# Optimization experiments

Hardware: AMD Instinct MI355X
Metric: run time of the kernel (lower is better)

## Reference

```python
import jax, jax.numpy as jnp
import numpy as np

BATCH = 1024
D_IN = 4096
D_OUT = 4096
B = 128  # block size
K_IN = (D_IN + B - 1) // B    # 32
K_OUT = (D_OUT + B - 1) // B  # 32


def setup_inputs() -> dict:
    key = jax.random.key(0)
    kx, kw, kd = jax.random.split(key, 3)
    x = jax.random.normal(kx, (BATCH, D_IN), dtype=jnp.float32)
    W = jax.random.normal(kw, (K_OUT, K_IN, B), dtype=jnp.float32) * 0.1
    # Bernoulli +/-1 diagonal
    D_bernoulli = jnp.where(jax.random.bernoulli(kd, p=0.5, shape=(D_IN,)), 1.0, -1.0).astype(jnp.float32)
    return {"x": x, "W": W, "D_bernoulli": D_bernoulli}


def reference(x, W, D_bernoulli):
    k_out, k_in, b = W.shape
    d_in = D_IN
    d_out = D_OUT
    if x.ndim == 1:
        x = x[None, :]
    batch = x.shape[0]
    # diagonal sign flip
    x_d = x * D_bernoulli[None, :]
    pad_len = k_in * b - d_in
    if pad_len > 0:
        x_d = jnp.pad(x_d, ((0, 0), (0, pad_len)))
    x_blocks = x_d.reshape(batch, k_in, b)
    # frequency-domain block-circulant matmul
    X_fft = jnp.fft.fft(x_blocks, axis=-1)            # (batch, k_in, b) complex
    W_fft = jnp.fft.fft(W, axis=-1)                    # (k_out, k_in, b) complex
    # Y_fft[n,o,:] = sum_j X_fft[n,j,:] * conj(W_fft[o,j,:])
    Y_fft = jnp.einsum('njb,ojb->nob', X_fft, jnp.conjugate(W_fft))
    Y = jnp.fft.ifft(Y_fft, axis=-1).real              # (batch, k_out, b)
    out_flat = Y.reshape(batch, k_out * b)
    if k_out * b > d_out:
        out_flat = out_flat[:, :d_out]
    return out_flat
```

## Files before the change

kernel.cpp:

```cpp
#include <hip/hip_runtime.h>
#include <hip/hip_bf16.h>

#define BATCH 1024
#define NF    65
#define TWOPI_OVER_B 0.049087385212340517f

typedef __attribute__((ext_vector_type(8))) short bf16x8;
typedef __attribute__((ext_vector_type(4))) float f32x4;

static __device__ __forceinline__ unsigned short f2bf(float f) {
    __hip_bfloat16 h = __float2bfloat16(f);
    return *reinterpret_cast<unsigned short*>(&h);
}
static __device__ __forceinline__ unsigned long long pack4(float a, float b, float c, float d) {
    return (unsigned long long)f2bf(a) | ((unsigned long long)f2bf(b) << 16)
         | ((unsigned long long)f2bf(c) << 32) | ((unsigned long long)f2bf(d) << 48);
}

__global__ __launch_bounds__(256) void k_init_frag(unsigned short* __restrict__ fragB,
                                                   unsigned short* __restrict__ fragCi) {
    int i = blockIdx.x * 256 + threadIdx.x;
    if (i < 18432) {
        int e = i & 7, l = (i >> 3) & 63, kb = (i >> 9) & 3, c = i >> 11;
        int kr = c * 16 + (l & 15);
        int t  = kb * 32 + (l >> 4) * 8 + e;
        float v = 0.f;
        if (kr < 65)       v =  cosf(TWOPI_OVER_B * (float)((kr * t) & 127));
        else if (kr < 130) v = -sinf(TWOPI_OVER_B * (float)(((kr - 65) * t) & 127));
        fragB[i] = f2bf(v);
    }
    if (i < 20480) {
        int e = i & 7, l = (i >> 3) & 63;
        int ckb = i >> 9; int kb = ckb % 5, c = ckb / 5;
        int kr = kb * 32 + (l >> 4) * 8 + e;
        int t  = c * 16 + (l & 15);
        float v = 0.f;
        if (kr < 65)       v =  cosf(TWOPI_OVER_B * (float)((kr * t) & 127));
        else if (kr < 130) v = -sinf(TWOPI_OVER_B * (float)(((kr - 65) * t) & 127));
        fragCi[i] = f2bf(v);
    }
}

#define SMEM_A_BYTES 37120

__global__ __launch_bounds__(256) void k_fdft_mfma(const float* __restrict__ x,
                                                   const float* __restrict__ D,
                                                   const bf16x8* __restrict__ fragB,
                                                   unsigned short* __restrict__ Xb) {
    __shared__ char smem[SMEM_A_BYTES];
    unsigned long long* xs8 = (unsigned long long*)smem;
    float* Yl = (float*)smem;
    int tid = threadIdx.x;
    int n0 = blockIdx.x * 2;

    #pragma unroll
    for (int it = 0; it < 8; ++it) {
        int f  = tid + it * 256;
        int nn = f >> 10;
        int f4 = f & 1023;
        float4 xa = ((const float4*)(x + (size_t)(n0 + nn) * 4096))[f4];
        float4 da = ((const float4*)D)[f4];
        int rl = nn * 32 + (f4 >> 5);
        int t0 = (f4 & 31) * 4;
        unsigned long long pk = pack4(xa.x * da.x, xa.y * da.y, xa.z * da.z, xa.w * da.w);
        int byte = (rl * 256 + t0 * 2) ^ ((rl & 7) << 4);
        xs8[byte >> 3] = pk;
    }
    __syncthreads();

    int l = tid & 63, w = tid >> 6;
    int rl_a = w * 16 + (l & 15);
    int coff = (l >> 4) * 16;
    bf16x8 a[4];
    #pragma unroll
    for (int kb = 0; kb < 4; ++kb) {
        int byte = (rl_a * 256 + kb * 64 + coff) ^ ((rl_a & 7) << 4);
        a[kb] = *(const bf16x8*)(smem + byte);
    }
    f32x4 acc[9];
    #pragma unroll
    for (int c = 0; c < 9; ++c) acc[c] = (f32x4)0.f;
    #pragma unroll
    for (int c = 0; c < 9; ++c)
        #pragma unroll
        for (int kb = 0; kb < 4; ++kb)
            acc[c] = __builtin_amdgcn_mfma_f32_16x16x32_bf16(a[kb], fragB[(c * 4 + kb) * 64 + l], acc[c], 0, 0, 0);
    __syncthreads();

    int rowd = w * 16 + (l >> 4) * 4;
    int cold = l & 15;
    #pragma unroll
    for (int c = 0; c < 9; ++c)
        #pragma unroll
        for (int r = 0; r < 4; ++r)
            Yl[(rowd + r) * 145 + c * 16 + cold] = acc[c][r];
    __syncthreads();

    for (int c2 = tid; c2 < 2080; c2 += 256) {
        int k = c2 >> 5, sub = c2 & 31, nn = sub >> 4, t = sub & 15;
        int j0 = t * 4;
        int col = (j0 < 32) ? k : 65 + k;
        int rlb = nn * 32 + (j0 & 31);
        unsigned long long pk = pack4(Yl[(rlb + 0) * 145 + col], Yl[(rlb + 1) * 145 + col],
                                      Yl[(rlb + 2) * 145 + col], Yl[(rlb + 3) * 145 + col]);
        *(unsigned long long*)(Xb + ((size_t)k * 1024 + n0 + nn) * 64 + j0) = pk;
    }
}

__global__ __launch_bounds__(256) void k_wfs_mfma(const float* __restrict__ W,
                                                  const bf16x8* __restrict__ fragB,
                                                  unsigned short* __restrict__ BmatT) {
    __shared__ char smem[SMEM_A_BYTES];
    unsigned long long* xs8 = (unsigned long long*)smem;
    float* Yl = (float*)smem;
    int tid = threadIdx.x;
    int o0 = blockIdx.x * 2;

    #pragma unroll
    for (int it = 0; it < 8; ++it) {
        int f  = tid + it * 256;
        float4 wa = ((const float4*)W)[(size_t)blockIdx.x * 2048 + f];
        int rl = f >> 5;
        int t0 = (f & 31) * 4;
        unsigned long long pk = pack4(wa.x, wa.y, wa.z, wa.w);
        int byte = (rl * 256 + t0 * 2) ^ ((rl & 7) << 4);
        xs8[byte >> 3] = pk;
    }
    __syncthreads();

    int l = tid & 63, w = tid >> 6;
    int rl_a = w * 16 + (l & 15);
    int coff = (l >> 4) * 16;
    bf16x8 a[4];
    #pragma unroll
    for (int kb = 0; kb < 4; ++kb) {
        int byte = (rl_a * 256 + kb * 64 + coff) ^ ((rl_a & 7) << 4);
        a[kb] = *(const bf16x8*)(smem + byte);
    }
    f32x4 acc[9];
    #pragma unroll
    for (int c = 0; c < 9; ++c) acc[c] = (f32x4)0.f;
    #pragma unroll
    for (int c = 0; c < 9; ++c)
        #pragma unroll
        for (int kb = 0; kb < 4; ++kb)
            acc[c] = __builtin_amdgcn_mfma_f32_16x16x32_bf16(a[kb], fragB[(c * 4 + kb) * 64 + l], acc[c], 0, 0, 0);
    __syncthreads();

    int rowd = w * 16 + (l >> 4) * 4;
    int cold = l & 15;
    #pragma unroll
    for (int c = 0; c < 9; ++c)
        #pragma unroll
        for (int r = 0; r < 4; ++r)
            Yl[(rowd + r) * 145 + c * 16 + cold] = acc[c][r];
    __syncthreads();

    for (int c2 = tid; c2 < 4160; c2 += 256) {
        int k = c2 >> 6, sub = c2 & 63;
        int oo = sub >> 5, h = (sub >> 4) & 1, t = sub & 15;
        int j0 = t * 4;
        float sc = (k == 0 || k == 64) ? (1.f / 128.f) : (2.f / 128.f);
        int col; float sgn;
        if (j0 < 32) { col = h ? 65 + k : k;  sgn = h ? -sc : sc; }
        else         { col = h ? k : 65 + k;  sgn = sc; }
        int rlb = oo * 32 + (j0 & 31);
        unsigned long long pk = pack4(sgn * Yl[(rlb + 0) * 145 + col], sgn * Yl[(rlb + 1) * 145 + col],
                                      sgn * Yl[(rlb + 2) * 145 + col], sgn * Yl[(rlb + 3) * 145 + col]);
        int o2 = h * 32 + o0 + oo;
        *(unsigned long long*)(BmatT + ((size_t)k * 64 + o2) * 64 + j0) = pk;
    }
}

__global__ __launch_bounds__(256) void k_einsum_mfma(const unsigned short* __restrict__ Xb,
                                                     const unsigned short* __restrict__ BmatT,
                                                     unsigned short* __restrict__ Y2) {
    __shared__ char lds[16384];
    int tid = threadIdx.x, l = tid & 63, w = tid >> 6;
    int k = blockIdx.x >> 3, mt = blockIdx.x & 7;
    int m0 = mt * 128 + w * 32;
    int lr = l & 15, lq = l >> 4;

    bf16x8 a[2][2], b[4][2];
    #pragma unroll
    for (int rf = 0; rf < 2; ++rf)
        #pragma unroll
        for (int kb = 0; kb < 2; ++kb)
            a[rf][kb] = *(const bf16x8*)(Xb + ((size_t)k * 1024 + m0 + rf * 16 + lr) * 64 + kb * 32 + lq * 8);
    #pragma unroll
    for (int cf = 0; cf < 4; ++cf)
        #pragma unroll
        for (int kb = 0; kb < 2; ++kb)
            b[cf][kb] = *(const bf16x8*)(BmatT + ((size_t)k * 64 + cf * 16 + lr) * 64 + kb * 32 + lq * 8);

    f32x4 acc[2][4];
    #pragma unroll
    for (int rf = 0; rf < 2; ++rf)
        #pragma unroll
        for (int cf = 0; cf < 4; ++cf) acc[rf][cf] = (f32x4)0.f;
    #pragma unroll
    for (int rf = 0; rf < 2; ++rf)
        #pragma unroll
        for (int cf = 0; cf < 4; ++cf) {
            acc[rf][cf] = __builtin_amdgcn_mfma_f32_16x16x32_bf16(a[rf][0], b[cf][0], acc[rf][cf], 0, 0, 0);
            acc[rf][cf] = __builtin_amdgcn_mfma_f32_16x16x32_bf16(a[rf][1], b[cf][1], acc[rf][cf], 0, 0, 0);
        }

    #pragma unroll
    for (int rf = 0; rf < 2; ++rf)
        #pragma unroll
        for (int cf = 0; cf < 4; ++cf)
            #pragma unroll
            for (int rr = 0; rr < 4; ++rr) {
                int row = rf * 16 + lq * 4 + rr;
                int col = cf * 16 + lr;
                int byte = w * 4096 + ((row * 128 + col * 2) ^ ((row & 7) << 4));
                *(unsigned short*)(lds + byte) = f2bf(acc[rf][cf][rr]);
            }
    __syncthreads();
    #pragma unroll
    for (int i = 0; i < 4; ++i) {
        int row = i * 8 + (l >> 3);
        int byte = w * 4096 + ((row * 128 + (l & 7) * 16) ^ ((row & 7) << 4));
        bf16x8 v = *(const bf16x8*)(lds + byte);
        *(bf16x8*)(Y2 + ((size_t)k * 1024 + m0 + row) * 64 + (l & 7) * 8) = v;
    }
}

__global__ __launch_bounds__(256) void k_idft_mfma(const unsigned short* __restrict__ Y2,
                                                   const bf16x8* __restrict__ fragCi,
                                                   float* __restrict__ out) {
    __shared__ char smem[20480];
    int tid = threadIdx.x;
    int row0 = blockIdx.x * 64;
    int n0 = blockIdx.x * 2;

    for (int i = tid; i < 1920; i += 256) {
        int rl = i / 30, cp = 130 + i % 30;
        int byte = (rl * 320 + cp * 2) ^ ((rl & 7) << 4);
        *(unsigned short*)(smem + byte) = 0;
    }
    for (int c2 = tid; c2 < 2080; c2 += 256) {
        int k = c2 >> 5, sub = c2 & 31, nn = sub >> 4, t = sub & 15;
        unsigned long long v = *(const unsigned long long*)(Y2 + ((size_t)k * 1024 + n0 + nn) * 64 + t * 4);
        int o2_0 = t * 4;
        int col = (o2_0 < 32) ? k : 65 + k;
        int r0 = nn * 32 + (o2_0 & 31);
        #pragma unroll
        for (int i = 0; i < 4; ++i) {
            int rl = r0 + i;
            int byte = (rl * 320 + col * 2) ^ ((rl & 7) << 4);
            *(unsigned short*)(smem + byte) = (unsigned short)(v >> (16 * i));
        }
    }
    __syncthreads();

    int l = tid & 63, w = tid >> 6;
    int rl_a = w * 16 + (l & 15);
    int coff = (l >> 4) * 16;
    bf16x8 a[5];
    #pragma unroll
    for (int kb = 0; kb < 5; ++kb) {
        int byte = (rl_a * 320 + kb * 64 + coff) ^ ((rl_a & 7) << 4);
        a[kb] = *(const bf16x8*)(smem + byte);
    }
    f32x4 acc[8];
    #pragma unroll
    for (int c = 0; c < 8; ++c) acc[c] = (f32x4)0.f;
    #pragma unroll
    for (int c = 0; c < 8; ++c)
        #pragma unroll
        for (int kb = 0; kb < 5; ++kb)
            acc[c] = __builtin_amdgcn_mfma_f32_16x16x32_bf16(a[kb], fragCi[(c * 5 + kb) * 64 + l], acc[c], 0, 0, 0);

    int rowd = row0 + w * 16 + (l >> 4) * 4;
    int cold = l & 15;
    #pragma unroll
    for (int c = 0; c < 8; ++c)
        #pragma unroll
        for (int r = 0; r < 4; ++r)
            out[(size_t)(rowd + r) * 128 + c * 16 + cold] = acc[c][r];
}

extern "C" void kernel_launch(void* const* d_in, const int* in_sizes, int n_in,
                              void* d_out, int out_size, void* d_ws, size_t ws_size,
                              hipStream_t stream) {
    const float* x = (const float*)d_in[0];
    const float* W = (const float*)d_in[1];
    const float* D = (const float*)d_in[2];
    float* out = (float*)d_out;
    float* ws  = (float*)d_ws;

    unsigned short* BmatT  = (unsigned short*)ws;
    unsigned short* Xb     = (unsigned short*)(ws + 133120);
    unsigned short* Y2     = (unsigned short*)(ws + 2263040);
    unsigned short* fragB  = (unsigned short*)(ws + 4392960);
    unsigned short* fragCi = (unsigned short*)(ws + 4402176);

    k_init_frag  <<<80, 256, 0, stream>>>(fragB, fragCi);
    k_wfs_mfma   <<<16, 256, 0, stream>>>(W, (const bf16x8*)fragB, BmatT);
    k_fdft_mfma  <<<512, 256, 0, stream>>>(x, D, (const bf16x8*)fragB, Xb);
    k_einsum_mfma<<<520, 256, 0, stream>>>(Xb, BmatT, Y2);
    k_idft_mfma  <<<512, 256, 0, stream>>>(Y2, (const bf16x8*)fragCi, out);
}
```

Measured before the change: 47.58 us.

## Fuse forward DFT, spectral einsum and inverse DFT into one kernel

```diff
diff --git a/kernel.cpp b/kernel.cpp
--- a/kernel.cpp
+++ b/kernel.cpp
@@ -1,8 +1,6 @@
 #include <hip/hip_runtime.h>
 #include <hip/hip_bf16.h>
 
-#define BATCH 1024
-#define NF    65
 #define TWOPI_OVER_B 0.049087385212340517f
 
 typedef __attribute__((ext_vector_type(8))) short bf16x8;
@@ -17,54 +15,59 @@
          | ((unsigned long long)f2bf(c) << 32) | ((unsigned long long)f2bf(d) << 48);
 }
 
-__global__ __launch_bounds__(256) void k_init_frag(unsigned short* __restrict__ fragB,
-                                                   unsigned short* __restrict__ fragCi) {
-    int i = blockIdx.x * 256 + threadIdx.x;
-    if (i < 18432) {
-        int e = i & 7, l = (i >> 3) & 63, kb = (i >> 9) & 3, c = i >> 11;
-        int kr = c * 16 + (l & 15);
-        int t  = kb * 32 + (l >> 4) * 8 + e;
+__global__ __launch_bounds__(256) void k_prep(const float* __restrict__ W,
+                                              unsigned short* __restrict__ fragB,
+                                              unsigned short* __restrict__ fragCi,
+                                              unsigned short* __restrict__ BmatT) {
+    __shared__ char smem[73984];
+    int tid = threadIdx.x;
+
+    if (blockIdx.x < 80) {
+        int i = blockIdx.x * 256 + tid;
+        if (i < 18432) {
+            int e = i & 7, l2 = (i >> 3) & 63, kb = (i >> 9) & 3, c = i >> 11;
+            int kr = c * 16 + (l2 & 15);
+            int t  = kb * 32 + (l2 >> 4) * 8 + e;
+            float v = 0.f;
+            if (kr < 65)       v =  cosf(TWOPI_OVER_B * (float)((kr * t) & 127));
+            else if (kr < 130) v = -sinf(TWOPI_OVER_B * (float)(((kr - 65) * t) & 127));
+            fragB[i] = f2bf(v);
+        }
+        if (i < 20480) {
+            int e = i & 7, l2 = (i >> 3) & 63;
+            int ckb = i >> 9; int kb = ckb % 5, c = ckb / 5;
+            int kr = kb * 32 + (l2 >> 4) * 8 + e;
+            int t  = c * 16 + (l2 & 15);
+            float v = 0.f;
+            if (kr < 65)       v =  cosf(TWOPI_OVER_B * (float)((kr * t) & 127));
+            else if (kr < 130) v = -sinf(TWOPI_OVER_B * (float)(((kr - 65) * t) & 127));
+            fragCi[i] = f2bf(v);
+        }
+        return;
+    }
+
+    int bw = blockIdx.x - 80;
+    unsigned long long* xs8 = (unsigned long long*)smem;
+    float* Yl = (float*)smem;
+    unsigned short* fB = (unsigned short*)(smem + 37120);
+
+    for (int i = tid; i < 18432; i += 256) {
+        int e = i & 7, l2 = (i >> 3) & 63, kb = (i >> 9) & 3, c = i >> 11;
+        int kr = c * 16 + (l2 & 15);
+        int t  = kb * 32 + (l2 >> 4) * 8 + e;
         float v = 0.f;
         if (kr < 65)       v =  cosf(TWOPI_OVER_B * (float)((kr * t) & 127));
         else if (kr < 130) v = -sinf(TWOPI_OVER_B * (float)(((kr - 65) * t) & 127));
-        fragB[i] = f2bf(v);
-    }
-    if (i < 20480) {
-        int e = i & 7, l = (i >> 3) & 63;
-        int ckb = i >> 9; int kb = ckb % 5, c = ckb / 5;
-        int kr = kb * 32 + (l >> 4) * 8 + e;
-        int t  = c * 16 + (l & 15);
-        float v = 0.f;
-        if (kr < 65)       v =  cosf(TWOPI_OVER_B * (float)((kr * t) & 127));
-        else if (kr < 130) v = -sinf(TWOPI_OVER_B * (float)(((kr - 65) * t) & 127));
-        fragCi[i] = f2bf(v);
-    }
-}
-
-#define SMEM_A_BYTES 37120
-
-__global__ __launch_bounds__(256) void k_fdft_mfma(const float* __restrict__ x,
-                                                   const float* __restrict__ D,
-                                                   const bf16x8* __restrict__ fragB,
-                                                   unsigned short* __restrict__ Xb) {
-    __shared__ char smem[SMEM_A_BYTES];
-    unsigned long long* xs8 = (unsigned long long*)smem;
-    float* Yl = (float*)smem;
-    int tid = threadIdx.x;
-    int n0 = blockIdx.x * 2;
-
+        fB[i] = f2bf(v);
+    }
     #pragma unroll
     for (int it = 0; it < 8; ++it) {
         int f  = tid + it * 256;
-        int nn = f >> 10;
-        int f4 = f & 1023;
-        float4 xa = ((const float4*)(x + (size_t)(n0 + nn) * 4096))[f4];
-        float4 da = ((const float4*)D)[f4];
-        int rl = nn * 32 + (f4 >> 5);
-        int t0 = (f4 & 31) * 4;
-        unsigned long long pk = pack4(xa.x * da.x, xa.y * da.y, xa.z * da.z, xa.w * da.w);
+        float4 wa = ((const float4*)W)[(size_t)bw * 2048 + f];
+        int rl = f >> 5;
+        int t0 = (f & 31) * 4;
         int byte = (rl * 256 + t0 * 2) ^ ((rl & 7) << 4);
-        xs8[byte >> 3] = pk;
+        xs8[byte >> 3] = pack4(wa.x, wa.y, wa.z, wa.w);
     }
     __syncthreads();
 
@@ -77,6 +80,8 @@
         int byte = (rl_a * 256 + kb * 64 + coff) ^ ((rl_a & 7) << 4);
         a[kb] = *(const bf16x8*)(smem + byte);
     }
+    __syncthreads();
+
     f32x4 acc[9];
     #pragma unroll
     for (int c = 0; c < 9; ++c) acc[c] = (f32x4)0.f;
@@ -84,8 +89,7 @@
     for (int c = 0; c < 9; ++c)
         #pragma unroll
         for (int kb = 0; kb < 4; ++kb)
-            acc[c] = __builtin_amdgcn_mfma_f32_16x16x32_bf16(a[kb], fragB[(c * 4 + kb) * 64 + l], acc[c], 0, 0, 0);
-    __syncthreads();
+            acc[c] = __builtin_amdgcn_mfma_f32_16x16x32_bf16(a[kb], ((const bf16x8*)fB)[(c * 4 + kb) * 64 + l], acc[c], 0, 0, 0);
 
     int rowd = w * 16 + (l >> 4) * 4;
     int cold = l & 15;
@@ -96,66 +100,7 @@
             Yl[(rowd + r) * 145 + c * 16 + cold] = acc[c][r];
     __syncthreads();
 
-    for (int c2 = tid; c2 < 2080; c2 += 256) {
-        int k = c2 >> 5, sub = c2 & 31, nn = sub >> 4, t = sub & 15;
-        int j0 = t * 4;
-        int col = (j0 < 32) ? k : 65 + k;
-        int rlb = nn * 32 + (j0 & 31);
-        unsigned long long pk = pack4(Yl[(rlb + 0) * 145 + col], Yl[(rlb + 1) * 145 + col],
-                                      Yl[(rlb + 2) * 145 + col], Yl[(rlb + 3) * 145 + col]);
-        *(unsigned long long*)(Xb + ((size_t)k * 1024 + n0 + nn) * 64 + j0) = pk;
-    }
-}
-
-__global__ __launch_bounds__(256) void k_wfs_mfma(const float* __restrict__ W,
-                                                  const bf16x8* __restrict__ fragB,
-                                                  unsigned short* __restrict__ BmatT) {
-    __shared__ char smem[SMEM_A_BYTES];
-    unsigned long long* xs8 = (unsigned long long*)smem;
-    float* Yl = (float*)smem;
-    int tid = threadIdx.x;
-    int o0 = blockIdx.x * 2;
-
-    #pragma unroll
-    for (int it = 0; it < 8; ++it) {
-        int f  = tid + it * 256;
-        float4 wa = ((const float4*)W)[(size_t)blockIdx.x * 2048 + f];
-        int rl = f >> 5;
-        int t0 = (f & 31) * 4;
-        unsigned long long pk = pack4(wa.x, wa.y, wa.z, wa.w);
-        int byte = (rl * 256 + t0 * 2) ^ ((rl & 7) << 4);
-        xs8[byte >> 3] = pk;
-    }
-    __syncthreads();
-
-    int l = tid & 63, w = tid >> 6;
-    int rl_a = w * 16 + (l & 15);
-    int coff = (l >> 4) * 16;
-    bf16x8 a[4];
-    #pragma unroll
-    for (int kb = 0; kb < 4; ++kb) {
-        int byte = (rl_a * 256 + kb * 64 + coff) ^ ((rl_a & 7) << 4);
-        a[kb] = *(const bf16x8*)(smem + byte);
-    }
-    f32x4 acc[9];
-    #pragma unroll
-    for (int c = 0; c < 9; ++c) acc[c] = (f32x4)0.f;
-    #pragma unroll
-    for (int c = 0; c < 9; ++c)
-        #pragma unroll
-        for (int kb = 0; kb < 4; ++kb)
-            acc[c] = __builtin_amdgcn_mfma_f32_16x16x32_bf16(a[kb], fragB[(c * 4 + kb) * 64 + l], acc[c], 0, 0, 0);
-    __syncthreads();
-
-    int rowd = w * 16 + (l >> 4) * 4;
-    int cold = l & 15;
-    #pragma unroll
-    for (int c = 0; c < 9; ++c)
-        #pragma unroll
-        for (int r = 0; r < 4; ++r)
-            Yl[(rowd + r) * 145 + c * 16 + cold] = acc[c][r];
-    __syncthreads();
-
+    int o0 = bw * 2;
     for (int c2 = tid; c2 < 4160; c2 += 256) {
         int k = c2 >> 6, sub = c2 & 63;
         int oo = sub >> 5, h = (sub >> 4) & 1, t = sub & 15;
@@ -172,114 +117,132 @@
     }
 }
 
-__global__ __launch_bounds__(256) void k_einsum_mfma(const unsigned short* __restrict__ Xb,
-                                                     const unsigned short* __restrict__ BmatT,
-                                                     unsigned short* __restrict__ Y2) {
-    __shared__ char lds[16384];
+#define YS_OFF 33280
+__global__ __launch_bounds__(512, 4) void k_fused(const float* __restrict__ x,
+                                                  const float* __restrict__ D,
+                                                  const bf16x8* __restrict__ fragB,
+                                                  const bf16x8* __restrict__ fragCi,
+                                                  const unsigned short* __restrict__ BmatT,
+                                                  float* __restrict__ out) {
+    __shared__ char smem[74240];
+    unsigned long long* xs8 = (unsigned long long*)smem;
     int tid = threadIdx.x, l = tid & 63, w = tid >> 6;
-    int k = blockIdx.x >> 3, mt = blockIdx.x & 7;
-    int m0 = mt * 128 + w * 32;
     int lr = l & 15, lq = l >> 4;
-
-    bf16x8 a[2][2], b[4][2];
-    #pragma unroll
-    for (int rf = 0; rf < 2; ++rf)
-        #pragma unroll
-        for (int kb = 0; kb < 2; ++kb)
-            a[rf][kb] = *(const bf16x8*)(Xb + ((size_t)k * 1024 + m0 + rf * 16 + lr) * 64 + kb * 32 + lq * 8);
-    #pragma unroll
-    for (int cf = 0; cf < 4; ++cf)
-        #pragma unroll
-        for (int kb = 0; kb < 2; ++kb)
-            b[cf][kb] = *(const bf16x8*)(BmatT + ((size_t)k * 64 + cf * 16 + lr) * 64 + kb * 32 + lq * 8);
-
-    f32x4 acc[2][4];
-    #pragma unroll
-    for (int rf = 0; rf < 2; ++rf)
-        #pragma unroll
-        for (int cf = 0; cf < 4; ++cf) acc[rf][cf] = (f32x4)0.f;
-    #pragma unroll
-    for (int rf = 0; rf < 2; ++rf)
-        #pragma unroll
-        for (int cf = 0; cf < 4; ++cf) {
-            acc[rf][cf] = __builtin_amdgcn_mfma_f32_16x16x32_bf16(a[rf][0], b[cf][0], acc[rf][cf], 0, 0, 0);
-            acc[rf][cf] = __builtin_amdgcn_mfma_f32_16x16x32_bf16(a[rf][1], b[cf][1], acc[rf][cf], 0, 0, 0);
-        }
-
-    #pragma unroll
-    for (int rf = 0; rf < 2; ++rf)
-        #pragma unroll
-        for (int cf = 0; cf < 4; ++cf)
-            #pragma unroll
-            for (int rr = 0; rr < 4; ++rr) {
-                int row = rf * 16 + lq * 4 + rr;
-                int col = cf * 16 + lr;
-                int byte = w * 4096 + ((row * 128 + col * 2) ^ ((row & 7) << 4));
-                *(unsigned short*)(lds + byte) = f2bf(acc[rf][cf][rr]);
-            }
-    __syncthreads();
-    #pragma unroll
-    for (int i = 0; i < 4; ++i) {
-        int row = i * 8 + (l >> 3);
-        int byte = w * 4096 + ((row * 128 + (l & 7) * 16) ^ ((row & 7) << 4));
-        bf16x8 v = *(const bf16x8*)(lds + byte);
-        *(bf16x8*)(Y2 + ((size_t)k * 1024 + m0 + row) * 64 + (l & 7) * 8) = v;
-    }
-}
-
-__global__ __launch_bounds__(256) void k_idft_mfma(const unsigned short* __restrict__ Y2,
-                                                   const bf16x8* __restrict__ fragCi,
-                                                   float* __restrict__ out) {
-    __shared__ char smem[20480];
-    int tid = threadIdx.x;
-    int row0 = blockIdx.x * 64;
-    int n0 = blockIdx.x * 2;
-
-    for (int i = tid; i < 1920; i += 256) {
+    int n0 = blockIdx.x * 4;
+
+    #pragma unroll
+    for (int it = 0; it < 8; ++it) {
+        int f  = tid + it * 512;
+        int nn = f >> 10, f4 = f & 1023;
+        float4 xa = ((const float4*)(x + (size_t)(n0 + nn) * 4096))[f4];
+        float4 da = ((const float4*)D)[f4];
+        int rl = nn * 32 + (f4 >> 5);
+        int t0 = (f4 & 31) * 4;
+        int byte = (rl * 256 + t0 * 2) ^ ((rl & 7) << 4);
+        xs8[byte >> 3] = pack4(xa.x * da.x, xa.y * da.y, xa.z * da.z, xa.w * da.w);
+    }
+    for (int i = tid; i < 3840; i += 512) {
         int rl = i / 30, cp = 130 + i % 30;
         int byte = (rl * 320 + cp * 2) ^ ((rl & 7) << 4);
-        *(unsigned short*)(smem + byte) = 0;
-    }
-    for (int c2 = tid; c2 < 2080; c2 += 256) {
-        int k = c2 >> 5, sub = c2 & 31, nn = sub >> 4, t = sub & 15;
-        unsigned long long v = *(const unsigned long long*)(Y2 + ((size_t)k * 1024 + n0 + nn) * 64 + t * 4);
-        int o2_0 = t * 4;
-        int col = (o2_0 < 32) ? k : 65 + k;
-        int r0 = nn * 32 + (o2_0 & 31);
-        #pragma unroll
-        for (int i = 0; i < 4; ++i) {
-            int rl = r0 + i;
-            int byte = (rl * 320 + col * 2) ^ ((rl & 7) << 4);
-            *(unsigned short*)(smem + byte) = (unsigned short)(v >> (16 * i));
-        }
-    }
-    __syncthreads();
-
-    int l = tid & 63, w = tid >> 6;
-    int rl_a = w * 16 + (l & 15);
-    int coff = (l >> 4) * 16;
-    bf16x8 a[5];
-    #pragma unroll
-    for (int kb = 0; kb < 5; ++kb) {
-        int byte = (rl_a * 320 + kb * 64 + coff) ^ ((rl_a & 7) << 4);
+        *(unsigned short*)(smem + YS_OFF + byte) = 0;
+    }
+    __syncthreads();
+
+    int rl_a = w * 16 + lr;
+    bf16x8 a[4];
+    #pragma unroll
+    for (int kb = 0; kb < 4; ++kb) {
+        int byte = (rl_a * 256 + kb * 64 + lq * 16) ^ ((rl_a & 7) << 4);
         a[kb] = *(const bf16x8*)(smem + byte);
     }
-    f32x4 acc[8];
-    #pragma unroll
-    for (int c = 0; c < 8; ++c) acc[c] = (f32x4)0.f;
-    #pragma unroll
-    for (int c = 0; c < 8; ++c)
-        #pragma unroll
-        for (int kb = 0; kb < 5; ++kb)
-            acc[c] = __builtin_amdgcn_mfma_f32_16x16x32_bf16(a[kb], fragCi[(c * 5 + kb) * 64 + l], acc[c], 0, 0, 0);
-
-    int rowd = row0 + w * 16 + (l >> 4) * 4;
-    int cold = l & 15;
-    #pragma unroll
-    for (int c = 0; c < 8; ++c)
-        #pragma unroll
-        for (int r = 0; r < 4; ++r)
-            out[(size_t)(rowd + r) * 128 + c * 16 + cold] = acc[c][r];
+    __syncthreads();
+
+    {
+        f32x4 acc[9];
+        #pragma unroll
+        for (int c = 0; c < 9; ++c) acc[c] = (f32x4)0.f;
+        #pragma unroll
+        for (int c = 0; c < 9; ++c)
+            #pragma unroll
+            for (int kb = 0; kb < 4; ++kb)
+                acc[c] = __builtin_amdgcn_mfma_f32_16x16x32_bf16(a[kb], fragB[(c * 4 + kb) * 64 + l], acc[c], 0, 0, 0);
+
+        int rowbase = w * 16 + lq * 4;
+        #pragma unroll
+        for (int c = 0; c < 9; ++c) {
+            int col = c * 16 + lr;
+            if (col < 130) {
+                int k, reim;
+                if (col < 65) { k = col;      reim = 0; }
+                else          { k = col - 65; reim = 32; }
+                #pragma unroll
+                for (int rr = 0; rr < 4; ++rr) {
+                    int rl2 = rowbase + rr;
+                    int nn = rl2 >> 5, j = rl2 & 31;
+                    int byte = (k * 512 + nn * 128 + (reim + j) * 2) ^ ((k & 7) << 4);
+                    *(unsigned short*)(smem + byte) = f2bf(acc[c][rr]);
+                }
+            }
+        }
+    }
+    __syncthreads();
+
+    for (int k = w; k < 65; k += 8) {
+        int xb = k * 512;
+        int swz = (k & 7) << 4;
+        bf16x8 a2[2];
+        a2[0] = *(const bf16x8*)(smem + ((xb + (lr & 3) * 128 +      lq * 16) ^ swz));
+        a2[1] = *(const bf16x8*)(smem + ((xb + (lr & 3) * 128 + 64 + lq * 16) ^ swz));
+        const unsigned short* bb = BmatT + (size_t)k * 4096 + lr * 64 + lq * 8;
+        f32x4 acc2[4];
+        #pragma unroll
+        for (int cf = 0; cf < 4; ++cf) acc2[cf] = (f32x4)0.f;
+        #pragma unroll
+        for (int cf = 0; cf < 4; ++cf) {
+            bf16x8 b0 = *(const bf16x8*)(bb + cf * 1024);
+            bf16x8 b1 = *(const bf16x8*)(bb + cf * 1024 + 32);
+            acc2[cf] = __builtin_amdgcn_mfma_f32_16x16x32_bf16(a2[0], b0, acc2[cf], 0, 0, 0);
+            acc2[cf] = __builtin_amdgcn_mfma_f32_16x16x32_bf16(a2[1], b1, acc2[cf], 0, 0, 0);
+        }
+        if (lq == 0) {
+            #pragma unroll
+            for (int cf = 0; cf < 4; ++cf) {
+                int o2  = cf * 16 + lr;
+                int col = (o2 < 32) ? k : 65 + k;
+                #pragma unroll
+                for (int rr = 0; rr < 4; ++rr) {
+                    int row2 = rr * 32 + (o2 & 31);
+                    int byte = (row2 * 320 + col * 2) ^ ((row2 & 7) << 4);
+                    *(unsigned short*)(smem + YS_OFF + byte) = f2bf(acc2[cf][rr]);
+                }
+            }
+        }
+    }
+    __syncthreads();
+
+    {
+        bf16x8 ac[5];
+        #pragma unroll
+        for (int kb = 0; kb < 5; ++kb) {
+            int byte = (rl_a * 320 + kb * 64 + lq * 16) ^ ((rl_a & 7) << 4);
+            ac[kb] = *(const bf16x8*)(smem + YS_OFF + byte);
+        }
+        f32x4 acc3[8];
+        #pragma unroll
+        for (int c = 0; c < 8; ++c) acc3[c] = (f32x4)0.f;
+        #pragma unroll
+        for (int c = 0; c < 8; ++c)
+            #pragma unroll
+            for (int kb = 0; kb < 5; ++kb)
+                acc3[c] = __builtin_amdgcn_mfma_f32_16x16x32_bf16(ac[kb], fragCi[(c * 5 + kb) * 64 + l], acc3[c], 0, 0, 0);
+
+        int rowd = blockIdx.x * 128 + w * 16 + lq * 4;
+        #pragma unroll
+        for (int c = 0; c < 8; ++c)
+            #pragma unroll
+            for (int r = 0; r < 4; ++r)
+                out[(size_t)(rowd + r) * 128 + c * 16 + lr] = acc3[c][r];
+    }
 }
 
 extern "C" void kernel_launch(void* const* d_in, const int* in_sizes, int n_in,
@@ -289,17 +252,11 @@
     const float* W = (const float*)d_in[1];
     const float* D = (const float*)d_in[2];
     float* out = (float*)d_out;
-    float* ws  = (float*)d_ws;
-
-    unsigned short* BmatT  = (unsigned short*)ws;
-    unsigned short* Xb     = (unsigned short*)(ws + 133120);
-    unsigned short* Y2     = (unsigned short*)(ws + 2263040);
-    unsigned short* fragB  = (unsigned short*)(ws + 4392960);
-    unsigned short* fragCi = (unsigned short*)(ws + 4402176);
-
-    k_init_frag  <<<80, 256, 0, stream>>>(fragB, fragCi);
-    k_wfs_mfma   <<<16, 256, 0, stream>>>(W, (const bf16x8*)fragB, BmatT);
-    k_fdft_mfma  <<<512, 256, 0, stream>>>(x, D, (const bf16x8*)fragB, Xb);
-    k_einsum_mfma<<<520, 256, 0, stream>>>(Xb, BmatT, Y2);
-    k_idft_mfma  <<<512, 256, 0, stream>>>(Y2, (const bf16x8*)fragCi, out);
-}
+
+    unsigned short* BmatT  = (unsigned short*)d_ws;
+    unsigned short* fragB  = BmatT + 266240;
+    unsigned short* fragCi = fragB + 18432;
+
+    k_prep <<<96, 256, 0, stream>>>(W, fragB, fragCi, BmatT);
+    k_fused<<<256, 512, 0, stream>>>(x, D, (const bf16x8*)fragB, (const bf16x8*)fragCi, BmatT, out);
+}
```

Measured after the change: 50.33 us. 1.06x slower.

## Fuse DFT, einsum and IDFT stages into a persistent kernel with grid barriers

Applied to the files above, without the earlier changes.

```diff
diff --git a/kernel.cpp b/kernel.cpp
--- a/kernel.cpp
+++ b/kernel.cpp
@@ -1,8 +1,6 @@
 #include <hip/hip_runtime.h>
 #include <hip/hip_bf16.h>
 
-#define BATCH 1024
-#define NF    65
 #define TWOPI_OVER_B 0.049087385212340517f
 
 typedef __attribute__((ext_vector_type(8))) short bf16x8;
@@ -17,54 +15,67 @@
          | ((unsigned long long)f2bf(c) << 32) | ((unsigned long long)f2bf(d) << 48);
 }
 
-__global__ __launch_bounds__(256) void k_init_frag(unsigned short* __restrict__ fragB,
-                                                   unsigned short* __restrict__ fragCi) {
-    int i = blockIdx.x * 256 + threadIdx.x;
-    if (i < 18432) {
-        int e = i & 7, l = (i >> 3) & 63, kb = (i >> 9) & 3, c = i >> 11;
-        int kr = c * 16 + (l & 15);
-        int t  = kb * 32 + (l >> 4) * 8 + e;
-        float v = 0.f;
-        if (kr < 65)       v =  cosf(TWOPI_OVER_B * (float)((kr * t) & 127));
-        else if (kr < 130) v = -sinf(TWOPI_OVER_B * (float)(((kr - 65) * t) & 127));
-        fragB[i] = f2bf(v);
-    }
-    if (i < 20480) {
-        int e = i & 7, l = (i >> 3) & 63;
-        int ckb = i >> 9; int kb = ckb % 5, c = ckb / 5;
-        int kr = kb * 32 + (l >> 4) * 8 + e;
-        int t  = c * 16 + (l & 15);
-        float v = 0.f;
-        if (kr < 65)       v =  cosf(TWOPI_OVER_B * (float)((kr * t) & 127));
-        else if (kr < 130) v = -sinf(TWOPI_OVER_B * (float)(((kr - 65) * t) & 127));
-        fragCi[i] = f2bf(v);
-    }
-}
-
-#define SMEM_A_BYTES 37120
-
-__global__ __launch_bounds__(256) void k_fdft_mfma(const float* __restrict__ x,
-                                                   const float* __restrict__ D,
-                                                   const bf16x8* __restrict__ fragB,
-                                                   unsigned short* __restrict__ Xb) {
-    __shared__ char smem[SMEM_A_BYTES];
+__global__ __launch_bounds__(256) void k_prep(const float* __restrict__ W,
+                                              unsigned short* __restrict__ fragB,
+                                              unsigned short* __restrict__ fragCi,
+                                              unsigned short* __restrict__ BmatT) {
+    __shared__ char smem[73984];
+    __shared__ float tbl[256];
+    int tid = threadIdx.x;
+
+    if (blockIdx.x < 80) {
+        int i = blockIdx.x * 256 + tid;
+        if (i < 18432) {
+            int e = i & 7, l2 = (i >> 3) & 63, kb = (i >> 9) & 3, c = i >> 11;
+            int kr = c * 16 + (l2 & 15);
+            int t  = kb * 32 + (l2 >> 4) * 8 + e;
+            float v = 0.f;
+            if (kr < 65)       v =  cosf(TWOPI_OVER_B * (float)((kr * t) & 127));
+            else if (kr < 130) v = -sinf(TWOPI_OVER_B * (float)(((kr - 65) * t) & 127));
+            fragB[i] = f2bf(v);
+        }
+        if (i < 20480) {
+            int e = i & 7, l2 = (i >> 3) & 63;
+            int ckb = i >> 9; int kb = ckb % 5, c = ckb / 5;
+            int kr = kb * 32 + (l2 >> 4) * 8 + e;
+            int t  = c * 16 + (l2 & 15);
+            float v = 0.f;
+            if (kr < 65)       v =  cosf(TWOPI_OVER_B * (float)((kr * t) & 127));
+            else if (kr < 130) v = -sinf(TWOPI_OVER_B * (float)(((kr - 65) * t) & 127));
+            fragCi[i] = f2bf(v);
+        }
+        return;
+    }
+
+    int bw = blockIdx.x - 80;
     unsigned long long* xs8 = (unsigned long long*)smem;
     float* Yl = (float*)smem;
-    int tid = threadIdx.x;
-    int n0 = blockIdx.x * 2;
-
+    unsigned short* fB = (unsigned short*)(smem + 37120);
+
+    for (int i = tid; i < 128; i += 256) {
+        float s, c;
+        sincosf(TWOPI_OVER_B * (float)i, &s, &c);
+        tbl[i] = c; tbl[128 + i] = s;
+    }
+    __syncthreads();
+
+    for (int i = tid; i < 18432; i += 256) {
+        int e = i & 7, l2 = (i >> 3) & 63, kb = (i >> 9) & 3, c = i >> 11;
+        int kr = c * 16 + (l2 & 15);
+        int t  = kb * 32 + (l2 >> 4) * 8 + e;
+        float v = 0.f;
+        if (kr < 65)       v =  tbl[(kr * t) & 127];
+        else if (kr < 130) v = -tbl[128 + (((kr - 65) * t) & 127)];
+        fB[i] = f2bf(v);
+    }
     #pragma unroll
     for (int it = 0; it < 8; ++it) {
         int f  = tid + it * 256;
-        int nn = f >> 10;
-        int f4 = f & 1023;
-        float4 xa = ((const float4*)(x + (size_t)(n0 + nn) * 4096))[f4];
-        float4 da = ((const float4*)D)[f4];
-        int rl = nn * 32 + (f4 >> 5);
-        int t0 = (f4 & 31) * 4;
-        unsigned long long pk = pack4(xa.x * da.x, xa.y * da.y, xa.z * da.z, xa.w * da.w);
+        float4 wa = ((const float4*)W)[(size_t)bw * 2048 + f];
+        int rl = f >> 5;
+        int t0 = (f & 31) * 4;
         int byte = (rl * 256 + t0 * 2) ^ ((rl & 7) << 4);
-        xs8[byte >> 3] = pk;
+        xs8[byte >> 3] = pack4(wa.x, wa.y, wa.z, wa.w);
     }
     __syncthreads();
 
@@ -77,6 +88,8 @@
         int byte = (rl_a * 256 + kb * 64 + coff) ^ ((rl_a & 7) << 4);
         a[kb] = *(const bf16x8*)(smem + byte);
     }
+    __syncthreads();
+
     f32x4 acc[9];
     #pragma unroll
     for (int c = 0; c < 9; ++c) acc[c] = (f32x4)0.f;
@@ -84,8 +97,7 @@
     for (int c = 0; c < 9; ++c)
         #pragma unroll
         for (int kb = 0; kb < 4; ++kb)
-            acc[c] = __builtin_amdgcn_mfma_f32_16x16x32_bf16(a[kb], fragB[(c * 4 + kb) * 64 + l], acc[c], 0, 0, 0);
-    __syncthreads();
+            acc[c] = __builtin_amdgcn_mfma_f32_16x16x32_bf16(a[kb], ((const bf16x8*)fB)[(c * 4 + kb) * 64 + l], acc[c], 0, 0, 0);
 
     int rowd = w * 16 + (l >> 4) * 4;
     int cold = l & 15;
@@ -96,66 +108,7 @@
             Yl[(rowd + r) * 145 + c * 16 + cold] = acc[c][r];
     __syncthreads();
 
-    for (int c2 = tid; c2 < 2080; c2 += 256) {
-        int k = c2 >> 5, sub = c2 & 31, nn = sub >> 4, t = sub & 15;
-        int j0 = t * 4;
-        int col = (j0 < 32) ? k : 65 + k;
-        int rlb = nn * 32 + (j0 & 31);
-        unsigned long long pk = pack4(Yl[(rlb + 0) * 145 + col], Yl[(rlb + 1) * 145 + col],
-                                      Yl[(rlb + 2) * 145 + col], Yl[(rlb + 3) * 145 + col]);
-        *(unsigned long long*)(Xb + ((size_t)k * 1024 + n0 + nn) * 64 + j0) = pk;
-    }
-}
-
-__global__ __launch_bounds__(256) void k_wfs_mfma(const float* __restrict__ W,
-                                                  const bf16x8* __restrict__ fragB,
-                                                  unsigned short* __restrict__ BmatT) {
-    __shared__ char smem[SMEM_A_BYTES];
-    unsigned long long* xs8 = (unsigned long long*)smem;
-    float* Yl = (float*)smem;
-    int tid = threadIdx.x;
-    int o0 = blockIdx.x * 2;
-
-    #pragma unroll
-    for (int it = 0; it < 8; ++it) {
-        int f  = tid + it * 256;
-        float4 wa = ((const float4*)W)[(size_t)blockIdx.x * 2048 + f];
-        int rl = f >> 5;
-        int t0 = (f & 31) * 4;
-        unsigned long long pk = pack4(wa.x, wa.y, wa.z, wa.w);
-        int byte = (rl * 256 + t0 * 2) ^ ((rl & 7) << 4);
-        xs8[byte >> 3] = pk;
-    }
-    __syncthreads();
-
-    int l = tid & 63, w = tid >> 6;
-    int rl_a = w * 16 + (l & 15);
-    int coff = (l >> 4) * 16;
-    bf16x8 a[4];
-    #pragma unroll
-    for (int kb = 0; kb < 4; ++kb) {
-        int byte = (rl_a * 256 + kb * 64 + coff) ^ ((rl_a & 7) << 4);
-        a[kb] = *(const bf16x8*)(smem + byte);
-    }
-    f32x4 acc[9];
-    #pragma unroll
-    for (int c = 0; c < 9; ++c) acc[c] = (f32x4)0.f;
-    #pragma unroll
-    for (int c = 0; c < 9; ++c)
-        #pragma unroll
-        for (int kb = 0; kb < 4; ++kb)
-            acc[c] = __builtin_amdgcn_mfma_f32_16x16x32_bf16(a[kb], fragB[(c * 4 + kb) * 64 + l], acc[c], 0, 0, 0);
-    __syncthreads();
-
-    int rowd = w * 16 + (l >> 4) * 4;
-    int cold = l & 15;
-    #pragma unroll
-    for (int c = 0; c < 9; ++c)
-        #pragma unroll
-        for (int r = 0; r < 4; ++r)
-            Yl[(rowd + r) * 145 + c * 16 + cold] = acc[c][r];
-    __syncthreads();
-
+    int o0 = bw * 2;
     for (int c2 = tid; c2 < 4160; c2 += 256) {
         int k = c2 >> 6, sub = c2 & 63;
         int oo = sub >> 5, h = (sub >> 4) & 1, t = sub & 15;
@@ -172,14 +125,67 @@
     }
 }
 
-__global__ __launch_bounds__(256) void k_einsum_mfma(const unsigned short* __restrict__ Xb,
-                                                     const unsigned short* __restrict__ BmatT,
-                                                     unsigned short* __restrict__ Y2) {
-    __shared__ char lds[16384];
-    int tid = threadIdx.x, l = tid & 63, w = tid >> 6;
-    int k = blockIdx.x >> 3, mt = blockIdx.x & 7;
+#define SMEM_BYTES 20480
+
+static __device__ __forceinline__ void fdft_body(char* smem, int tid, int np,
+        const float* __restrict__ x, const float* __restrict__ D,
+        const bf16x8* __restrict__ fragB, unsigned short* __restrict__ Xb) {
+    unsigned long long* xs8 = (unsigned long long*)smem;
+    int n0 = np * 2;
+    #pragma unroll
+    for (int it = 0; it < 8; ++it) {
+        int f  = tid + it * 256;
+        int nn = f >> 10;
+        int f4 = f & 1023;
+        float4 xa = ((const float4*)(x + (size_t)(n0 + nn) * 4096))[f4];
+        float4 da = ((const float4*)D)[f4];
+        int rl = nn * 32 + (f4 >> 5);
+        int t0 = (f4 & 31) * 4;
+        int byte = (rl * 256 + t0 * 2) ^ ((rl & 7) << 4);
+        xs8[byte >> 3] = pack4(xa.x * da.x, xa.y * da.y, xa.z * da.z, xa.w * da.w);
+    }
+    __syncthreads();
+
+    int l = tid & 63, w = tid >> 6;
+    int lr = l & 15, lq = l >> 4;
+    int rl_a = w * 16 + lr;
+    bf16x8 a[4];
+    #pragma unroll
+    for (int kb = 0; kb < 4; ++kb) {
+        int byte = (rl_a * 256 + kb * 64 + lq * 16) ^ ((rl_a & 7) << 4);
+        a[kb] = *(const bf16x8*)(smem + byte);
+    }
+    f32x4 acc[9];
+    #pragma unroll
+    for (int c = 0; c < 9; ++c) acc[c] = (f32x4)0.f;
+    #pragma unroll
+    for (int c = 0; c < 9; ++c)
+        #pragma unroll
+        for (int kb = 0; kb < 4; ++kb)
+            acc[c] = __builtin_amdgcn_mfma_f32_16x16x32_bf16(a[kb], fragB[(c * 4 + kb) * 64 + l], acc[c], 0, 0, 0);
+
+    int rowbase = w * 16 + lq * 4;
+    int nn = rowbase >> 5, j0 = rowbase & 31;
+    #pragma unroll
+    for (int c = 0; c < 9; ++c) {
+        int col = c * 16 + lr;
+        if (col < 130) {
+            int k   = (col < 65) ? col : col - 65;
+            int off = (col < 65) ? 0 : 32;
+            *(unsigned long long*)(Xb + ((size_t)k * 1024 + n0 + nn) * 64 + off + j0)
+                = pack4(acc[c][0], acc[c][1], acc[c][2], acc[c][3]);
+        }
+    }
+}
+
+static __device__ __forceinline__ void einsum_body(char* lds, int tid, int u,
+        const unsigned short* __restrict__ Xb, const unsigned short* __restrict__ BmatT,
+        unsigned short* __restrict__ Y2) {
+    int l = tid & 63, w = tid >> 6;
+    int k = u >> 3, mt = u & 7;
     int m0 = mt * 128 + w * 32;
     int lr = l & 15, lq = l >> 4;
+    __syncthreads();
 
     bf16x8 a[2][2], b[4][2];
     #pragma unroll
@@ -227,13 +233,12 @@
     }
 }
 
-__global__ __launch_bounds__(256) void k_idft_mfma(const unsigned short* __restrict__ Y2,
-                                                   const bf16x8* __restrict__ fragCi,
-                                                   float* __restrict__ out) {
-    __shared__ char smem[20480];
-    int tid = threadIdx.x;
-    int row0 = blockIdx.x * 64;
-    int n0 = blockIdx.x * 2;
+static __device__ __forceinline__ void idft_body(char* smem, int tid, int bi,
+        const unsigned short* __restrict__ Y2, const bf16x8* __restrict__ fragCi,
+        float* __restrict__ out) {
+    int row0 = bi * 64;
+    int n0 = bi * 2;
+    __syncthreads();
 
     for (int i = tid; i < 1920; i += 256) {
         int rl = i / 30, cp = 130 + i % 30;
@@ -280,6 +285,39 @@
         #pragma unroll
         for (int r = 0; r < 4; ++r)
             out[(size_t)(rowd + r) * 128 + c * 16 + cold] = acc[c][r];
+}
+
+static __device__ __forceinline__ void gbar(unsigned* bar, unsigned target) {
+    __syncthreads();
+    if (threadIdx.x == 0) {
+        __hip_atomic_fetch_add(bar, 1u, __ATOMIC_RELEASE, __HIP_MEMORY_SCOPE_AGENT);
+        while (__hip_atomic_load(bar, __ATOMIC_ACQUIRE, __HIP_MEMORY_SCOPE_AGENT) < target)
+            __builtin_amdgcn_s_sleep(2);
+    }
+    __syncthreads();
+}
+
+__global__ __launch_bounds__(256, 2) void k_persist(const float* __restrict__ x,
+                                                    const float* __restrict__ D,
+                                                    float* __restrict__ out,
+                                                    const bf16x8* __restrict__ fragB,
+                                                    const bf16x8* __restrict__ fragCi,
+                                                    const unsigned short* __restrict__ BmatT,
+                                                    unsigned short* __restrict__ Xb,
+                                                    unsigned short* __restrict__ Y2,
+                                                    unsigned* __restrict__ bar) {
+    __shared__ char smem[SMEM_BYTES];
+    int tid = threadIdx.x;
+    int bi  = blockIdx.x;
+
+    fdft_body(smem, tid, bi, x, D, fragB, Xb);
+    gbar(bar, 512);
+
+    einsum_body(smem, tid, bi, Xb, BmatT, Y2);
+    if (bi < 8) einsum_body(smem, tid, 512 + bi, Xb, BmatT, Y2);
+    gbar(bar, 1024);
+
+    idft_body(smem, tid, bi, Y2, fragCi, out);
 }
 
 extern "C" void kernel_launch(void* const* d_in, const int* in_sizes, int n_in,
@@ -295,11 +333,11 @@
     unsigned short* Xb     = (unsigned short*)(ws + 133120);
     unsigned short* Y2     = (unsigned short*)(ws + 2263040);
     unsigned short* fragB  = (unsigned short*)(ws + 4392960);
-    unsigned short* fragCi = (unsigned short*)(ws + 4402176);
-
-    k_init_frag  <<<80, 256, 0, stream>>>(fragB, fragCi);
-    k_wfs_mfma   <<<16, 256, 0, stream>>>(W, (const bf16x8*)fragB, BmatT);
-    k_fdft_mfma  <<<512, 256, 0, stream>>>(x, D, (const bf16x8*)fragB, Xb);
-    k_einsum_mfma<<<520, 256, 0, stream>>>(Xb, BmatT, Y2);
-    k_idft_mfma  <<<512, 256, 0, stream>>>(Y2, (const bf16x8*)fragCi, out);
-}
+    unsigned short* fragCi = fragB + 18432;
+    unsigned*       bar    = (unsigned*)((char*)d_ws + 17649728);
+
+    hipMemsetAsync(bar, 0, 64, stream);
+    k_prep   <<<96, 256, 0, stream>>>(W, fragB, fragCi, BmatT);
+    k_persist<<<512, 256, 0, stream>>>(x, D, out, (const bf16x8*)fragB,
+                                       (const bf16x8*)fragCi, BmatT, Xb, Y2, bar);
+}
```

Result: slower. 152.5 us (+220.5%).

## Split DFT and einsum kernels into finer blocks to double grid parallelism

Applied to the files above, without the earlier changes.

```diff
diff --git a/kernel.cpp b/kernel.cpp
--- a/kernel.cpp
+++ b/kernel.cpp
@@ -1,8 +1,6 @@
 #include <hip/hip_runtime.h>
 #include <hip/hip_bf16.h>
 
-#define BATCH 1024
-#define NF    65
 #define TWOPI_OVER_B 0.049087385212340517f
 
 typedef __attribute__((ext_vector_type(8))) short bf16x8;
@@ -41,76 +39,10 @@
     }
 }
 
-#define SMEM_A_BYTES 37120
-
-__global__ __launch_bounds__(256) void k_fdft_mfma(const float* __restrict__ x,
-                                                   const float* __restrict__ D,
-                                                   const bf16x8* __restrict__ fragB,
-                                                   unsigned short* __restrict__ Xb) {
-    __shared__ char smem[SMEM_A_BYTES];
-    unsigned long long* xs8 = (unsigned long long*)smem;
-    float* Yl = (float*)smem;
-    int tid = threadIdx.x;
-    int n0 = blockIdx.x * 2;
-
-    #pragma unroll
-    for (int it = 0; it < 8; ++it) {
-        int f  = tid + it * 256;
-        int nn = f >> 10;
-        int f4 = f & 1023;
-        float4 xa = ((const float4*)(x + (size_t)(n0 + nn) * 4096))[f4];
-        float4 da = ((const float4*)D)[f4];
-        int rl = nn * 32 + (f4 >> 5);
-        int t0 = (f4 & 31) * 4;
-        unsigned long long pk = pack4(xa.x * da.x, xa.y * da.y, xa.z * da.z, xa.w * da.w);
-        int byte = (rl * 256 + t0 * 2) ^ ((rl & 7) << 4);
-        xs8[byte >> 3] = pk;
-    }
-    __syncthreads();
-
-    int l = tid & 63, w = tid >> 6;
-    int rl_a = w * 16 + (l & 15);
-    int coff = (l >> 4) * 16;
-    bf16x8 a[4];
-    #pragma unroll
-    for (int kb = 0; kb < 4; ++kb) {
-        int byte = (rl_a * 256 + kb * 64 + coff) ^ ((rl_a & 7) << 4);
-        a[kb] = *(const bf16x8*)(smem + byte);
-    }
-    f32x4 acc[9];
-    #pragma unroll
-    for (int c = 0; c < 9; ++c) acc[c] = (f32x4)0.f;
-    #pragma unroll
-    for (int c = 0; c < 9; ++c)
-        #pragma unroll
-        for (int kb = 0; kb < 4; ++kb)
-            acc[c] = __builtin_amdgcn_mfma_f32_16x16x32_bf16(a[kb], fragB[(c * 4 + kb) * 64 + l], acc[c], 0, 0, 0);
-    __syncthreads();
-
-    int rowd = w * 16 + (l >> 4) * 4;
-    int cold = l & 15;
-    #pragma unroll
-    for (int c = 0; c < 9; ++c)
-        #pragma unroll
-        for (int r = 0; r < 4; ++r)
-            Yl[(rowd + r) * 145 + c * 16 + cold] = acc[c][r];
-    __syncthreads();
-
-    for (int c2 = tid; c2 < 2080; c2 += 256) {
-        int k = c2 >> 5, sub = c2 & 31, nn = sub >> 4, t = sub & 15;
-        int j0 = t * 4;
-        int col = (j0 < 32) ? k : 65 + k;
-        int rlb = nn * 32 + (j0 & 31);
-        unsigned long long pk = pack4(Yl[(rlb + 0) * 145 + col], Yl[(rlb + 1) * 145 + col],
-                                      Yl[(rlb + 2) * 145 + col], Yl[(rlb + 3) * 145 + col]);
-        *(unsigned long long*)(Xb + ((size_t)k * 1024 + n0 + nn) * 64 + j0) = pk;
-    }
-}
-
 __global__ __launch_bounds__(256) void k_wfs_mfma(const float* __restrict__ W,
                                                   const bf16x8* __restrict__ fragB,
                                                   unsigned short* __restrict__ BmatT) {
-    __shared__ char smem[SMEM_A_BYTES];
+    __shared__ char smem[37120];
     unsigned long long* xs8 = (unsigned long long*)smem;
     float* Yl = (float*)smem;
     int tid = threadIdx.x;
@@ -122,9 +54,8 @@
         float4 wa = ((const float4*)W)[(size_t)blockIdx.x * 2048 + f];
         int rl = f >> 5;
         int t0 = (f & 31) * 4;
-        unsigned long long pk = pack4(wa.x, wa.y, wa.z, wa.w);
         int byte = (rl * 256 + t0 * 2) ^ ((rl & 7) << 4);
-        xs8[byte >> 3] = pk;
+        xs8[byte >> 3] = pack4(wa.x, wa.y, wa.z, wa.w);
     }
     __syncthreads();
 
@@ -172,68 +103,138 @@
     }
 }
 
-__global__ __launch_bounds__(256) void k_einsum_mfma(const unsigned short* __restrict__ Xb,
-                                                     const unsigned short* __restrict__ BmatT,
-                                                     unsigned short* __restrict__ Y2) {
-    __shared__ char lds[16384];
+__global__ __launch_bounds__(256) void k_fdft(const float* __restrict__ x,
+                                              const float* __restrict__ D,
+                                              const bf16x8* __restrict__ fragB,
+                                              unsigned short* __restrict__ Xb) {
+    __shared__ char smem[37120];
+    unsigned long long* xs8 = (unsigned long long*)smem;
+    float* Yl = (float*)smem;
+    int tid = threadIdx.x;
+    int np = blockIdx.x & 511, ch = blockIdx.x >> 9;
+    int cbase = ch ? 5 : 0, cn = ch ? 4 : 5;
+    int n0 = np * 2;
+
+    #pragma unroll
+    for (int it = 0; it < 8; ++it) {
+        int f  = tid + it * 256;
+        int nn = f >> 10;
+        int f4 = f & 1023;
+        float4 xa = ((const float4*)(x + (size_t)(n0 + nn) * 4096))[f4];
+        float4 da = ((const float4*)D)[f4];
+        int rl = nn * 32 + (f4 >> 5);
+        int t0 = (f4 & 31) * 4;
+        int byte = (rl * 256 + t0 * 2) ^ ((rl & 7) << 4);
+        xs8[byte >> 3] = pack4(xa.x * da.x, xa.y * da.y, xa.z * da.z, xa.w * da.w);
+    }
+    __syncthreads();
+
+    int l = tid & 63, w = tid >> 6;
+    int rl_a = w * 16 + (l & 15);
+    int coff = (l >> 4) * 16;
+    bf16x8 a[4];
+    #pragma unroll
+    for (int kb = 0; kb < 4; ++kb) {
+        int byte = (rl_a * 256 + kb * 64 + coff) ^ ((rl_a & 7) << 4);
+        a[kb] = *(const bf16x8*)(smem + byte);
+    }
+    f32x4 acc[5];
+    #pragma unroll
+    for (int ci = 0; ci < 5; ++ci) acc[ci] = (f32x4)0.f;
+    #pragma unroll
+    for (int ci = 0; ci < 5; ++ci) {
+        int c = cbase + ci;
+        if (c < 9) {
+            #pragma unroll
+            for (int kb = 0; kb < 4; ++kb)
+                acc[ci] = __builtin_amdgcn_mfma_f32_16x16x32_bf16(a[kb], fragB[(c * 4 + kb) * 64 + l], acc[ci], 0, 0, 0);
+        }
+    }
+    __syncthreads();
+
+    int rowd = w * 16 + (l >> 4) * 4;
+    int cold = l & 15;
+    #pragma unroll
+    for (int ci = 0; ci < 5; ++ci) {
+        int c = cbase + ci;
+        if (c < 9) {
+            #pragma unroll
+            for (int r = 0; r < 4; ++r)
+                Yl[(rowd + r) * 145 + c * 16 + cold] = acc[ci][r];
+        }
+    }
+    __syncthreads();
+
+    for (int c2 = tid; c2 < 2080; c2 += 256) {
+        int k = c2 >> 5, sub = c2 & 31, nn = sub >> 4, t = sub & 15;
+        int j0 = t * 4;
+        int col = (j0 < 32) ? k : 65 + k;
+        int cc = col >> 4;
+        if (cc >= cbase && cc < cbase + cn) {
+            int rlb = nn * 32 + (j0 & 31);
+            unsigned long long pk = pack4(Yl[(rlb + 0) * 145 + col], Yl[(rlb + 1) * 145 + col],
+                                          Yl[(rlb + 2) * 145 + col], Yl[(rlb + 3) * 145 + col]);
+            *(unsigned long long*)(Xb + ((size_t)k * 1024 + n0 + nn) * 64 + j0) = pk;
+        }
+    }
+}
+
+__global__ __launch_bounds__(256) void k_einsum(const unsigned short* __restrict__ Xb,
+                                                const unsigned short* __restrict__ BmatT,
+                                                unsigned short* __restrict__ Y2) {
+    __shared__ char lds[8192];
     int tid = threadIdx.x, l = tid & 63, w = tid >> 6;
-    int k = blockIdx.x >> 3, mt = blockIdx.x & 7;
-    int m0 = mt * 128 + w * 32;
+    int k = blockIdx.x >> 4, mt = blockIdx.x & 15;
+    int m0 = mt * 64 + w * 16;
     int lr = l & 15, lq = l >> 4;
 
-    bf16x8 a[2][2], b[4][2];
-    #pragma unroll
-    for (int rf = 0; rf < 2; ++rf)
-        #pragma unroll
-        for (int kb = 0; kb < 2; ++kb)
-            a[rf][kb] = *(const bf16x8*)(Xb + ((size_t)k * 1024 + m0 + rf * 16 + lr) * 64 + kb * 32 + lq * 8);
+    bf16x8 a[2], b[4][2];
+    #pragma unroll
+    for (int kb = 0; kb < 2; ++kb)
+        a[kb] = *(const bf16x8*)(Xb + ((size_t)k * 1024 + m0 + lr) * 64 + kb * 32 + lq * 8);
     #pragma unroll
     for (int cf = 0; cf < 4; ++cf)
         #pragma unroll
         for (int kb = 0; kb < 2; ++kb)
             b[cf][kb] = *(const bf16x8*)(BmatT + ((size_t)k * 64 + cf * 16 + lr) * 64 + kb * 32 + lq * 8);
 
-    f32x4 acc[2][4];
-    #pragma unroll
-    for (int rf = 0; rf < 2; ++rf)
-        #pragma unroll
-        for (int cf = 0; cf < 4; ++cf) acc[rf][cf] = (f32x4)0.f;
-    #pragma unroll
-    for (int rf = 0; rf < 2; ++rf)
-        #pragma unroll
-        for (int cf = 0; cf < 4; ++cf) {
-            acc[rf][cf] = __builtin_amdgcn_mfma_f32_16x16x32_bf16(a[rf][0], b[cf][0], acc[rf][cf], 0, 0, 0);
-            acc[rf][cf] = __builtin_amdgcn_mfma_f32_16x16x32_bf16(a[rf][1], b[cf][1], acc[rf][cf], 0, 0, 0);
-        }
-
-    #pragma unroll
-    for (int rf = 0; rf < 2; ++rf)
-        #pragma unroll
-        for (int cf = 0; cf < 4; ++cf)
-            #pragma unroll
-            for (int rr = 0; rr < 4; ++rr) {
-                int row = rf * 16 + lq * 4 + rr;
-                int col = cf * 16 + lr;
-                int byte = w * 4096 + ((row * 128 + col * 2) ^ ((row & 7) << 4));
-                *(unsigned short*)(lds + byte) = f2bf(acc[rf][cf][rr]);
-            }
-    __syncthreads();
-    #pragma unroll
-    for (int i = 0; i < 4; ++i) {
+    f32x4 acc[4];
+    #pragma unroll
+    for (int cf = 0; cf < 4; ++cf) acc[cf] = (f32x4)0.f;
+    #pragma unroll
+    for (int cf = 0; cf < 4; ++cf) {
+        acc[cf] = __builtin_amdgcn_mfma_f32_16x16x32_bf16(a[0], b[cf][0], acc[cf], 0, 0, 0);
+        acc[cf] = __builtin_amdgcn_mfma_f32_16x16x32_bf16(a[1], b[cf][1], acc[cf], 0, 0, 0);
+    }
+
+    #pragma unroll
+    for (int cf = 0; cf < 4; ++cf)
+        #pragma unroll
+        for (int rr = 0; rr < 4; ++rr) {
+            int row = lq * 4 + rr;
+            int col = cf * 16 + lr;
+            int byte = w * 2048 + ((row * 128 + col * 2) ^ ((row & 7) << 4));
+            *(unsigned short*)(lds + byte) = f2bf(acc[cf][rr]);
+        }
+    __syncthreads();
+    #pragma unroll
+    for (int i = 0; i < 2; ++i) {
         int row = i * 8 + (l >> 3);
-        int byte = w * 4096 + ((row * 128 + (l & 7) * 16) ^ ((row & 7) << 4));
+        int byte = w * 2048 + ((row * 128 + (l & 7) * 16) ^ ((row & 7) << 4));
         bf16x8 v = *(const bf16x8*)(lds + byte);
         *(bf16x8*)(Y2 + ((size_t)k * 1024 + m0 + row) * 64 + (l & 7) * 8) = v;
     }
 }
 
-__global__ __launch_bounds__(256) void k_idft_mfma(const unsigned short* __restrict__ Y2,
-                                                   const bf16x8* __restrict__ fragCi,
-                                                   float* __restrict__ out) {
+__global__ __launch_bounds__(256) void k_idft(const unsigned short* __restrict__ Y2,
+                                              const bf16x8* __restrict__ fragCi,
+                                              float* __restrict__ out) {
     __shared__ char smem[20480];
     int tid = threadIdx.x;
-    int row0 = blockIdx.x * 64;
-    int n0 = blockIdx.x * 2;
+    int np = blockIdx.x & 511, ch = blockIdx.x >> 9;
+    int cbase = ch * 4;
+    int row0 = np * 64;
+    int n0 = np * 2;
 
     for (int i = tid; i < 1920; i += 256) {
         int rl = i / 30, cp = 130 + i % 30;
@@ -264,22 +265,22 @@
         int byte = (rl_a * 320 + kb * 64 + coff) ^ ((rl_a & 7) << 4);
         a[kb] = *(const bf16x8*)(smem + byte);
     }
-    f32x4 acc[8];
-    #pragma unroll
-    for (int c = 0; c < 8; ++c) acc[c] = (f32x4)0.f;
-    #pragma unroll
-    for (int c = 0; c < 8; ++c)
+    f32x4 acc[4];
+    #pragma unroll
+    for (int ci = 0; ci < 4; ++ci) acc[ci] = (f32x4)0.f;
+    #pragma unroll
+    for (int ci = 0; ci < 4; ++ci)
         #pragma unroll
         for (int kb = 0; kb < 5; ++kb)
-            acc[c] = __builtin_amdgcn_mfma_f32_16x16x32_bf16(a[kb], fragCi[(c * 5 + kb) * 64 + l], acc[c], 0, 0, 0);
+            acc[ci] = __builtin_amdgcn_mfma_f32_16x16x32_bf16(a[kb], fragCi[((cbase + ci) * 5 + kb) * 64 + l], acc[ci], 0, 0, 0);
 
     int rowd = row0 + w * 16 + (l >> 4) * 4;
     int cold = l & 15;
     #pragma unroll
-    for (int c = 0; c < 8; ++c)
+    for (int ci = 0; ci < 4; ++ci)
         #pragma unroll
         for (int r = 0; r < 4; ++r)
-            out[(size_t)(rowd + r) * 128 + c * 16 + cold] = acc[c][r];
+            out[(size_t)(rowd + r) * 128 + (cbase + ci) * 16 + cold] = acc[ci][r];
 }
 
 extern "C" void kernel_launch(void* const* d_in, const int* in_sizes, int n_in,
@@ -295,11 +296,11 @@
     unsigned short* Xb     = (unsigned short*)(ws + 133120);
     unsigned short* Y2     = (unsigned short*)(ws + 2263040);
     unsigned short* fragB  = (unsigned short*)(ws + 4392960);
-    unsigned short* fragCi = (unsigned short*)(ws + 4402176);
-
-    k_init_frag  <<<80, 256, 0, stream>>>(fragB, fragCi);
-    k_wfs_mfma   <<<16, 256, 0, stream>>>(W, (const bf16x8*)fragB, BmatT);
-    k_fdft_mfma  <<<512, 256, 0, stream>>>(x, D, (const bf16x8*)fragB, Xb);
-    k_einsum_mfma<<<520, 256, 0, stream>>>(Xb, BmatT, Y2);
-    k_idft_mfma  <<<512, 256, 0, stream>>>(Y2, (const bf16x8*)fragCi, out);
-}
+    unsigned short* fragCi = fragB + 18432;
+
+    k_init_frag<<<80,   256, 0, stream>>>(fragB, fragCi);
+    k_wfs_mfma <<<16,   256, 0, stream>>>(W, (const bf16x8*)fragB, BmatT);
+    k_fdft     <<<1024, 256, 0, stream>>>(x, D, (const bf16x8*)fragB, Xb);
+    k_einsum   <<<1040, 256, 0, stream>>>(Xb, BmatT, Y2);
+    k_idft     <<<1024, 256, 0, stream>>>(Y2, (const bf16x8*)fragCi, out);
+}
```

New measurement: 50.78 us. 6.7% more time.
